# Kernel tuning notes

Hardware: AMD Instinct MI355X
Metric: run time of the kernel (lower is better)

## Reference

```python
import jax, jax.numpy as jnp
import numpy as np

B, C, D_EMB = 512, 100000, 128
SCALE = 3.0
EPS = 1e-5


def _l2norm(x, eps=1e-12):
    # matches torch F.normalize(p=2, dim=-1)
    n = jnp.sqrt(jnp.sum(x * x, axis=-1, keepdims=True))
    return x / jnp.maximum(n, eps)


def setup_inputs() -> dict:
    key = jax.random.key(0)
    k1, k2, k3 = jax.random.split(key, 3)
    X = jax.random.normal(k1, (B, D_EMB), dtype=jnp.float32)
    indices = jnp.arange(B, dtype=jnp.int64)
    T = jax.random.randint(k2, (B,), 0, C).astype(jnp.int64)
    proxies = jax.random.normal(k3, (C, D_EMB), dtype=jnp.float32) / 8.0
    return {"X": X, "indices": indices, "T": T, "proxies": proxies}


def reference(X, indices, T, proxies):
    P = _l2norm(proxies)            # (C, D)
    Xn = _l2norm(X)                 # (B, D)

    # cross_attention -----------------------------------------------------
    Pb = P[T]                       # (B, D) gather of class proxies
    # affinity2boundary[b,k] = relu(<(Pb[b]+Pb[k])/2, Xn[k]>)
    #   = relu(0.5 * ((Pb @ Xn.T)[b,k] + diag[k]))  -- avoids (B,B,D) intermediate
    diag = jnp.sum(Pb * Xn, axis=-1)                       # (B,)
    aff2b = jax.nn.relu(0.5 * (Pb @ Xn.T + diag[None, :]))  # (B, B)
    aff2x = jax.nn.relu(Xn @ Xn.T)                          # (B, B)
    attention = aff2b + aff2x

    # NOTE: faithful to torch broadcasting: (B,B) / (B,) divides by COLUMN sums
    attention = attention / (attention.sum(-1) + EPS)       # (B, B)
    attention_weights = attention @ Xn                      # (B, D)
    X2 = Xn + attention_weights

    Ps = SCALE * _l2norm(P)         # (C, D), rows have norm SCALE
    Xs = SCALE * _l2norm(X2)        # (B, D)

    # squared pairwise distance block between X rows and proxy rows
    sx = jnp.sum(Xs * Xs, axis=-1)  # (B,)
    sp = jnp.sum(Ps * Ps, axis=-1)  # (C,)
    Dm = jnp.maximum(sx[:, None] + sp[None, :] - 2.0 * (Xs @ Ps.T), 0.0)  # (B, C)

    # one-hot targets (smoothing_const = 0) with masked log-softmax
    lsm = jax.nn.log_softmax(-Dm, axis=-1)                  # (B, C)
    loss = -lsm[jnp.arange(B), T]                           # (B,)
    return loss.mean()
```

## Files before the change

### kernel.cpp

```cpp
#include <hip/hip_runtime.h>
#include <hip/hip_bf16.h>
#include <math.h>

#define B_N 512
#define C_N 100000
#define CPAD 100032
#define D_N 128
#define NCHUNK (CPAD / 64)

typedef short short8 __attribute__((ext_vector_type(8)));
typedef float f32x4 __attribute__((ext_vector_type(4)));

__device__ __forceinline__ unsigned short f2bf(float f) {
  unsigned int u = __float_as_uint(f);
  u += 0x7fffu + ((u >> 16) & 1u);
  return (unsigned short)(u >> 16);
}

__device__ __forceinline__ void gl_lds16(const void* g, void* l) {
  __builtin_amdgcn_global_load_lds(
      (const __attribute__((address_space(1))) void*)g,
      (__attribute__((address_space(3))) void*)l, 16, 0, 0);
}

template <int NT>
__device__ __forceinline__ float block_reduce_sum(float v, float* red) {
  int t = threadIdx.x;
  __syncthreads();
  red[t] = v;
  __syncthreads();
#pragma unroll
  for (int s = NT / 2; s > 0; s >>= 1) {
    if (t < s) red[t] += red[t + s];
    __syncthreads();
  }
  return red[0];
}

__global__ void k12_norm(const float* __restrict__ X, const float* __restrict__ proxies,
                         const int* __restrict__ T, float* __restrict__ Xn,
                         float* __restrict__ Pb, float* __restrict__ diagv) {
  __shared__ float red[128];
  int b = blockIdx.x, t = threadIdx.x;
  float v = X[b * D_N + t];
  float ss = block_reduce_sum<128>(v * v, red);
  float xn = v / fmaxf(sqrtf(ss), 1e-12f);
  Xn[b * D_N + t] = xn;
  int row = T[b];
  float p = proxies[(size_t)row * D_N + t];
  float ss2 = block_reduce_sum<128>(p * p, red);
  float pn = p / fmaxf(sqrtf(ss2), 1e-12f);
  Pb[b * D_N + t] = pn;
  float d = block_reduce_sum<128>(pn * xn, red);
  if (t == 0) diagv[b] = d;
}

__global__ __launch_bounds__(256) void k3_att(const float* __restrict__ Xn,
                                              const float* __restrict__ Pb,
                                              const float* __restrict__ diagv,
                                              float* __restrict__ A, float* __restrict__ S) {
  __shared__ float xb[128], pbv[128];
  __shared__ float red[256];
  int b = blockIdx.x, t = threadIdx.x;
  if (t < 128) {
    xb[t] = Xn[b * D_N + t];
    pbv[t] = Pb[b * D_N + t];
  }
  __syncthreads();
  float rs = 0.f;
  for (int k = t; k < B_N; k += 256) {
    const float4* xr = (const float4*)(Xn + (size_t)k * D_N);
    float d1 = 0.f, d2 = 0.f;
#pragma unroll
    for (int i = 0; i < 32; i++) {
      float4 v = xr[i];
      d1 += pbv[4 * i] * v.x + pbv[4 * i + 1] * v.y + pbv[4 * i + 2] * v.z + pbv[4 * i + 3] * v.w;
      d2 += xb[4 * i] * v.x + xb[4 * i + 1] * v.y + xb[4 * i + 2] * v.z + xb[4 * i + 3] * v.w;
    }
    float a = fmaxf(0.5f * (d1 + diagv[k]), 0.f) + fmaxf(d2, 0.f);
    A[(size_t)b * B_N + k] = a;
    rs += a;
  }
  rs = block_reduce_sum<256>(rs, red);
  if (t == 0) S[b] = rs;
}

__global__ void k4a_aw(const float* __restrict__ Xn, const float* __restrict__ A,
                       const float* __restrict__ S, float* __restrict__ X2) {
  __shared__ float aw[128];
  int b = blockIdx.x, t = threadIdx.x;
  int k0 = blockIdx.y * 128;
  aw[t] = A[(size_t)b * B_N + k0 + t] / (S[k0 + t] + 1e-5f);
  __syncthreads();
  float acc = 0.f;
#pragma unroll 16
  for (int kk = 0; kk < 128; kk++) acc += aw[kk] * Xn[(size_t)(k0 + kk) * D_N + t];
  atomicAdd(&X2[b * D_N + t], acc);
}

__global__ void k4b_xs(const float* __restrict__ Xn, const float* __restrict__ X2,
                       const float* __restrict__ Pb, unsigned short* __restrict__ Xsb,
                       float* __restrict__ lossT) {
  __shared__ float red[128];
  int b = blockIdx.x, t = threadIdx.x;
  float x2 = Xn[b * D_N + t] + X2[b * D_N + t];
  float ss = block_reduce_sum<128>(x2 * x2, red);
  float xs = 3.f * x2 / fmaxf(sqrtf(ss), 1e-12f);
  Xsb[b * D_N + t] = f2bf(xs);
  float dt = block_reduce_sum<128>(xs * Pb[b * D_N + t], red);
  if (t == 0) lossT[b] = fmaxf(18.f - 6.f * dt, 0.f);
}

__global__ __launch_bounds__(256) void k5_pn(const float* __restrict__ proxies,
                                             unsigned short* __restrict__ Pnb) {
  int t = threadIdx.x;
  int lane = t & 63;
  int row = blockIdx.x * 4 + (t >> 6);
  float2 v = make_float2(0.f, 0.f);
  if (row < C_N) v = *(const float2*)(proxies + (size_t)row * D_N + 2 * lane);
  float ss = v.x * v.x + v.y * v.y;
#pragma unroll
  for (int off = 1; off < 64; off <<= 1) ss += __shfl_xor(ss, off);
  float inv = 1.f / fmaxf(sqrtf(ss), 1e-12f);
  unsigned short a = f2bf(v.x * inv), b = f2bf(v.y * inv);
  unsigned int pk = (unsigned int)a | ((unsigned int)b << 16);
  *(unsigned int*)(Pnb + (size_t)row * D_N + 2 * lane) = pk;
}

__global__ __launch_bounds__(256, 4) void k6_big(const unsigned short* __restrict__ Pnb,
                                                 const unsigned short* __restrict__ Xsb,
                                                 float* __restrict__ sumexpP) {
  __shared__ __align__(16) unsigned short sP[2][64 * 128];
  const int t = threadIdx.x;
  const int w = t >> 6;
  const int lane = t & 63;
  const int lc = lane & 15;
  const int q = lane >> 4;
  const int b0 = blockIdx.y * 128;

  short8 afr[2][4];
#pragma unroll
  for (int mt = 0; mt < 2; mt++)
#pragma unroll
    for (int ks = 0; ks < 4; ks++)
      afr[mt][ks] = *(const short8*)(Xsb + (size_t)(b0 + 32 * w + 16 * mt + lc) * D_N +
                                     ks * 32 + q * 8);

  float pe[2][4];
#pragma unroll
  for (int mt = 0; mt < 2; mt++)
#pragma unroll
    for (int r = 0; r < 4; r++) pe[mt][r] = 0.f;

  const int rR = 16 * w + (lane >> 4);
  const int gsrc0 = (lane & 15);
#define STAGE(c0_, buf_)                                                              \
  {                                                                                   \
    _Pragma("unroll") for (int j = 0; j < 4; j++) {                                   \
      int R = rR + 4 * j;                                                             \
      int g = gsrc0 ^ ((R)&15);                                                       \
      gl_lds16(Pnb + (((size_t)(c0_) + R) << 7) + (g << 3),                           \
               &sP[buf_][w * 2048 + j * 512]);                                        \
    }                                                                                 \
  }

  int cc = blockIdx.x;
  STAGE(cc * 64, 0);
  int buf = 0;
  while (true) {
    __syncthreads();
    int nc = cc + gridDim.x;
    if (nc < NCHUNK) STAGE(nc * 64, buf ^ 1);

    const int c0 = cc * 64;
    f32x4 acc[2][4];
#pragma unroll
    for (int mt = 0; mt < 2; mt++)
#pragma unroll
      for (int nt = 0; nt < 4; nt++) acc[mt][nt] = (f32x4){0.f, 0.f, 0.f, 0.f};

#pragma unroll
    for (int ks = 0; ks < 4; ks++) {
      short8 bfr[4];
#pragma unroll
      for (int nt = 0; nt < 4; nt++) {
        int R = 16 * nt + lc;
        int g = (ks * 4 + q) ^ lc;
        bfr[nt] = *(const short8*)(&sP[buf][R * 128 + (g << 3)]);
      }
#pragma unroll
      for (int nt = 0; nt < 4; nt++)
#pragma unroll
        for (int mt = 0; mt < 2; mt++)
          acc[mt][nt] = __builtin_amdgcn_mfma_f32_16x16x32_bf16(afr[mt][ks], bfr[nt],
                                                                acc[mt][nt], 0, 0, 0);
    }

#pragma unroll
    for (int mt = 0; mt < 2; mt++) {
#pragma unroll
      for (int nt = 0; nt < 4; nt++) {
        bool ok = (c0 + 16 * nt + lc) < C_N;
        f32x4 a = acc[mt][nt];
#pragma unroll
        for (int r = 0; r < 4; r++) {
          float e = __expf(fminf(6.f * a[r] - 18.f, 0.f));
          pe[mt][r] += ok ? e : 0.f;
        }
      }
    }
    if (nc >= NCHUNK) break;
    cc = nc;
    buf ^= 1;
  }

#pragma unroll
  for (int mt = 0; mt < 2; mt++) {
#pragma unroll
    for (int r = 0; r < 4; r++) {
      float p = pe[mt][r];
      p += __shfl_xor(p, 1);
      p += __shfl_xor(p, 2);
      p += __shfl_xor(p, 4);
      p += __shfl_xor(p, 8);
      if (lc == 0) {
        int rb = b0 + 32 * w + 16 * mt + 4 * q + r;
        atomicAdd(&sumexpP[rb * 16], p);
      }
    }
  }
}

__global__ void k7_final(const float* __restrict__ lossT, const float* __restrict__ sumexpP,
                         float* __restrict__ out) {
  __shared__ float red[512];
  int t = threadIdx.x;
  float v = lossT[t] + logf(sumexpP[t * 16]);
  float s = block_reduce_sum<512>(v, red);
  if (t == 0) out[0] = s * (1.0f / 512.0f);
}

extern "C" void kernel_launch(void* const* d_in, const int* in_sizes, int n_in,
                              void* d_out, int out_size, void* d_ws, size_t ws_size,
                              hipStream_t stream) {
  const float* X = (const float*)d_in[0];
  const int* T = (const int*)d_in[2];
  const float* proxies = (const float*)d_in[3];
  float* out = (float*)d_out;

  char* ws = (char*)d_ws;
  unsigned short* Pnb = (unsigned short*)ws;
  float* Xn = (float*)(ws + (size_t)CPAD * D_N * 2);
  float* Pb = Xn + B_N * D_N;
  float* X2 = Pb + B_N * D_N;
  float* dg = X2 + B_N * D_N;
  float* S = dg + B_N;
  float* lossT = S + B_N;
  float* sumexpP = lossT + B_N;
  unsigned short* Xsb = (unsigned short*)(sumexpP + B_N * 16);
  float* A = (float*)(Xsb + B_N * D_N);

  hipMemsetAsync(X2, 0, B_N * D_N * sizeof(float), stream);
  hipMemsetAsync(sumexpP, 0, B_N * 16 * sizeof(float), stream);
  k5_pn<<<CPAD / 4, 256, 0, stream>>>(proxies, Pnb);
  k12_norm<<<B_N, 128, 0, stream>>>(X, proxies, T, Xn, Pb, dg);
  k3_att<<<B_N, 256, 0, stream>>>(Xn, Pb, dg, A, S);
  k4a_aw<<<dim3(B_N, 4), 128, 0, stream>>>(Xn, A, S, X2);
  k4b_xs<<<B_N, 128, 0, stream>>>(Xn, X2, Pb, Xsb, lossT);
  k6_big<<<dim3(256, 4), 256, 0, stream>>>(Pnb, Xsb, sumexpP);
  k7_final<<<1, 512, 0, stream>>>(lossT, sumexpP, out);
}
```

Measured before the change: 167.0 us.

## Fuse prep kernels, drop memsets, add dynamic chunk scheduling and last-block final reduce

Merges the proxy normalization and the X/proxy-gather normalization into one launch, and zeroes X2 and sumexpP inside kernels so the two memset calls go away. The big GEMM kernel now pulls chunks from per-row-group atomic counters instead of a fixed stride, and the last block to finish does the final loss reduction, which removes the separate final kernel. This cuts launch count and evens out load across blocks. The cost is atomic traffic on every chunk fetch and a threadfence-based last-block pattern that relies on correct memory ordering.

```diff
diff --git a/kernel.cpp b/kernel.cpp
--- a/kernel.cpp
+++ b/kernel.cpp
@@ -7,6 +7,10 @@
 #define CPAD 100032
 #define D_N 128
 #define NCHUNK (CPAD / 64)
+#define K5_BLOCKS (CPAD / 4)
+#define K6_GX 256
+#define K6_GY 4
+#define K6_BLOCKS (K6_GX * K6_GY)
 
 typedef short short8 __attribute__((ext_vector_type(8)));
 typedef float f32x4 __attribute__((ext_vector_type(4)));
@@ -37,22 +41,45 @@
   return red[0];
 }
 
-__global__ void k12_norm(const float* __restrict__ X, const float* __restrict__ proxies,
-                         const int* __restrict__ T, float* __restrict__ Xn,
-                         float* __restrict__ Pb, float* __restrict__ diagv) {
-  __shared__ float red[128];
-  int b = blockIdx.x, t = threadIdx.x;
-  float v = X[b * D_N + t];
-  float ss = block_reduce_sum<128>(v * v, red);
-  float xn = v / fmaxf(sqrtf(ss), 1e-12f);
-  Xn[b * D_N + t] = xn;
-  int row = T[b];
-  float p = proxies[(size_t)row * D_N + t];
-  float ss2 = block_reduce_sum<128>(p * p, red);
-  float pn = p / fmaxf(sqrtf(ss2), 1e-12f);
-  Pb[b * D_N + t] = pn;
-  float d = block_reduce_sum<128>(pn * xn, red);
-  if (t == 0) diagv[b] = d;
+__global__ __launch_bounds__(256) void kA(const float* __restrict__ X,
+                                          const float* __restrict__ proxies,
+                                          const int* __restrict__ T,
+                                          float* __restrict__ Xn, float* __restrict__ Pb,
+                                          float* __restrict__ diagv, float* __restrict__ X2,
+                                          unsigned short* __restrict__ Pnb) {
+  int bid = blockIdx.x;
+  int t = threadIdx.x;
+  if (bid < K5_BLOCKS) {
+    int lane = t & 63;
+    int row = bid * 4 + (t >> 6);
+    float2 v = make_float2(0.f, 0.f);
+    if (row < C_N) v = *(const float2*)(proxies + (size_t)row * D_N + 2 * lane);
+    float ss = v.x * v.x + v.y * v.y;
+#pragma unroll
+    for (int off = 1; off < 64; off <<= 1) ss += __shfl_xor(ss, off);
+    float inv = 1.f / fmaxf(sqrtf(ss), 1e-12f);
+    unsigned short a = f2bf(v.x * inv), b = f2bf(v.y * inv);
+    unsigned int pk = (unsigned int)a | ((unsigned int)b << 16);
+    *(unsigned int*)(Pnb + (size_t)row * D_N + 2 * lane) = pk;
+  } else {
+    __shared__ float red[256];
+    int b = bid - K5_BLOCKS;
+    bool act = t < D_N;
+    float v = act ? X[b * D_N + t] : 0.f;
+    float ss = block_reduce_sum<256>(v * v, red);
+    float xn = v / fmaxf(sqrtf(ss), 1e-12f);
+    if (act) {
+      Xn[b * D_N + t] = xn;
+      X2[b * D_N + t] = 0.f;
+    }
+    int row = T[b];
+    float p = act ? proxies[(size_t)row * D_N + t] : 0.f;
+    float ss2 = block_reduce_sum<256>(p * p, red);
+    float pn = p / fmaxf(sqrtf(ss2), 1e-12f);
+    if (act) Pb[b * D_N + t] = pn;
+    float d = block_reduce_sum<256>(pn * xn, red);
+    if (t == 0) diagv[b] = d;
+  }
 }
 
 __global__ __launch_bounds__(256) void k3_att(const float* __restrict__ Xn,
@@ -100,7 +127,8 @@
 
 __global__ void k4b_xs(const float* __restrict__ Xn, const float* __restrict__ X2,
                        const float* __restrict__ Pb, unsigned short* __restrict__ Xsb,
-                       float* __restrict__ lossT) {
+                       float* __restrict__ lossT, float* __restrict__ sumexpP,
+                       int* __restrict__ ctrs) {
   __shared__ float red[128];
   int b = blockIdx.x, t = threadIdx.x;
   float x2 = Xn[b * D_N + t] + X2[b * D_N + t];
@@ -108,35 +136,32 @@
   float xs = 3.f * x2 / fmaxf(sqrtf(ss), 1e-12f);
   Xsb[b * D_N + t] = f2bf(xs);
   float dt = block_reduce_sum<128>(xs * Pb[b * D_N + t], red);
-  if (t == 0) lossT[b] = fmaxf(18.f - 6.f * dt, 0.f);
-}
-
-__global__ __launch_bounds__(256) void k5_pn(const float* __restrict__ proxies,
-                                             unsigned short* __restrict__ Pnb) {
-  int t = threadIdx.x;
-  int lane = t & 63;
-  int row = blockIdx.x * 4 + (t >> 6);
-  float2 v = make_float2(0.f, 0.f);
-  if (row < C_N) v = *(const float2*)(proxies + (size_t)row * D_N + 2 * lane);
-  float ss = v.x * v.x + v.y * v.y;
-#pragma unroll
-  for (int off = 1; off < 64; off <<= 1) ss += __shfl_xor(ss, off);
-  float inv = 1.f / fmaxf(sqrtf(ss), 1e-12f);
-  unsigned short a = f2bf(v.x * inv), b = f2bf(v.y * inv);
-  unsigned int pk = (unsigned int)a | ((unsigned int)b << 16);
-  *(unsigned int*)(Pnb + (size_t)row * D_N + 2 * lane) = pk;
+  if (t == 0) {
+    lossT[b] = fmaxf(18.f - 6.f * dt, 0.f);
+    sumexpP[b * 16] = 0.f;
+    if (b == 0) {
+      ctrs[0] = K6_GX; ctrs[1] = K6_GX; ctrs[2] = K6_GX; ctrs[3] = K6_GX;
+      ctrs[4] = 0;
+    }
+  }
 }
 
 __global__ __launch_bounds__(256, 4) void k6_big(const unsigned short* __restrict__ Pnb,
                                                  const unsigned short* __restrict__ Xsb,
-                                                 float* __restrict__ sumexpP) {
+                                                 float* __restrict__ sumexpP,
+                                                 const float* __restrict__ lossT,
+                                                 int* __restrict__ ctrs,
+                                                 float* __restrict__ out) {
   __shared__ __align__(16) unsigned short sP[2][64 * 128];
+  __shared__ int sTk[2];
+  __shared__ float redf[256];
   const int t = threadIdx.x;
   const int w = t >> 6;
   const int lane = t & 63;
   const int lc = lane & 15;
   const int q = lane >> 4;
   const int b0 = blockIdx.y * 128;
+  int* myctr = &ctrs[blockIdx.y];
 
   short8 afr[2][4];
 #pragma unroll
@@ -166,11 +191,13 @@
 
   int cc = blockIdx.x;
   STAGE(cc * 64, 0);
+  if (t == 0) sTk[1] = atomicAdd(myctr, 1);
   int buf = 0;
   while (true) {
     __syncthreads();
-    int nc = cc + gridDim.x;
+    int nc = sTk[buf ^ 1];
     if (nc < NCHUNK) STAGE(nc * 64, buf ^ 1);
+    if (t == 0) sTk[buf] = atomicAdd(myctr, 1);
 
     const int c0 = cc * 64;
     f32x4 acc[2][4];
@@ -229,15 +256,24 @@
       }
     }
   }
-}
-
-__global__ void k7_final(const float* __restrict__ lossT, const float* __restrict__ sumexpP,
-                         float* __restrict__ out) {
-  __shared__ float red[512];
-  int t = threadIdx.x;
-  float v = lossT[t] + logf(sumexpP[t * 16]);
-  float s = block_reduce_sum<512>(v, red);
-  if (t == 0) out[0] = s * (1.0f / 512.0f);
+
+  __threadfence();
+  __shared__ int sLast;
+  if (t == 0) sLast = atomicAdd(&ctrs[4], 1);
+  __syncthreads();
+  if (sLast == K6_BLOCKS - 1) {
+    __threadfence();
+    float v = 0.f;
+#pragma unroll
+    for (int i = 0; i < 2; i++) {
+      int b = t + 256 * i;
+      float se = __hip_atomic_load(&sumexpP[b * 16], __ATOMIC_RELAXED,
+                                   __HIP_MEMORY_SCOPE_AGENT);
+      v += lossT[b] + logf(se);
+    }
+    float s = block_reduce_sum<256>(v, redf);
+    if (t == 0) out[0] = s * (1.0f / 512.0f);
+  }
 }
 
 extern "C" void kernel_launch(void* const* d_in, const int* in_sizes, int n_in,
@@ -259,14 +295,11 @@
   float* sumexpP = lossT + B_N;
   unsigned short* Xsb = (unsigned short*)(sumexpP + B_N * 16);
   float* A = (float*)(Xsb + B_N * D_N);
-
-  hipMemsetAsync(X2, 0, B_N * D_N * sizeof(float), stream);
-  hipMemsetAsync(sumexpP, 0, B_N * 16 * sizeof(float), stream);
-  k5_pn<<<CPAD / 4, 256, 0, stream>>>(proxies, Pnb);
-  k12_norm<<<B_N, 128, 0, stream>>>(X, proxies, T, Xn, Pb, dg);
+  int* ctrs = (int*)(A + B_N * B_N);
+
+  kA<<<K5_BLOCKS + B_N, 256, 0, stream>>>(X, proxies, T, Xn, Pb, dg, X2, Pnb);
   k3_att<<<B_N, 256, 0, stream>>>(Xn, Pb, dg, A, S);
   k4a_aw<<<dim3(B_N, 4), 128, 0, stream>>>(Xn, A, S, X2);
-  k4b_xs<<<B_N, 128, 0, stream>>>(Xn, X2, Pb, Xsb, lossT);
-  k6_big<<<dim3(256, 4), 256, 0, stream>>>(Pnb, Xsb, sumexpP);
-  k7_final<<<1, 512, 0, stream>>>(lossT, sumexpP, out);
-}
+  k4b_xs<<<B_N, 128, 0, stream>>>(Xn, X2, Pb, Xsb, lossT, sumexpP, ctrs);
+  k6_big<<<dim3(K6_GX, K6_GY), 256, 0, stream>>>(Pnb, Xsb, sumexpP, lossT, ctrs, out);
+}
```

New measurement: 286.2 us. 1.71x slower.
